# Performance work log

Measured on AMD Instinct MI355X. Metric: run time of the kernel, lower is better.

Reference implementation:

```python
import jax, jax.numpy as jnp
import numpy as np

B, S, D, H, L, V = 2, 1024, 512, 8, 4, 32000
DK = D // H
EPS = 1e-6


def _positional_encoding():
    # row i of the original (d_model, seq) array: sin if i even else cos of t/10000^(2i/D); transposed -> (S, D)
    i = jnp.arange(D, dtype=jnp.float32)
    ang = jnp.arange(S, dtype=jnp.float32)[:, None] / (10000.0 ** (2.0 * i / D))[None, :]
    return jnp.where((jnp.arange(D) % 2 == 0)[None, :], jnp.sin(ang), jnp.cos(ang))


def _layernorm(x, g, b):
    m = jnp.mean(x, axis=-1, keepdims=True)
    s = jnp.std(x, axis=-1, keepdims=True)
    return g / (s + EPS) * (x - m) + b


def _mha(x, wq, wk, wv, wo, mask):
    # wq/wk/wv: [H, D, DK]; all heads batched via einsum (equivalent to per-head loop + concat)
    q = jnp.einsum('bsd,hdk->bhsk', x, wq)
    k = jnp.einsum('bsd,hdk->bhsk', x, wk)
    v = jnp.einsum('bsd,hdk->bhsk', x, wv)
    scores = jnp.einsum('bhsk,bhtk->bhst', q, k) / np.float32(np.sqrt(DK))
    if mask is not None:
        scores = scores + mask  # additive upper-tri 1e-15, faithful to source
    attn = jax.nn.softmax(scores, axis=-1)
    o = jnp.einsum('bhst,bhtv->bhsv', attn, v)
    o = o.transpose(0, 2, 1, 3).reshape(B, S, D)  # concat heads
    return o @ wo


def setup_inputs() -> dict:
    key = jax.random.key(0)
    ks = jax.random.split(key, 13)
    n = lambda k, shape, s=0.05: jax.random.normal(k, shape, dtype=jnp.float32) * s
    return {
        'tokens': jax.random.randint(ks[0], (B, S), 0, V),
        'emb': n(ks[1], (V, D)),
        'Wq': n(ks[2], (L, 2, H, D, DK)),
        'Wk': n(ks[3], (L, 2, H, D, DK)),
        'Wv': n(ks[4], (L, 2, H, D, DK)),
        'Wo': n(ks[5], (L, 2, D, D)),
        'ln_gain': 1.0 + n(ks[6], (L, 3, S, D)),
        'ln_bias': n(ks[7], (L, 3, S, D)),
        'ffn_w1': n(ks[8], (L, D, D)),
        'ffn_b1': n(ks[9], (L, D)),
        'ffn_w2': n(ks[10], (L, D, D)),
        'ffn_b2': n(ks[11], (L, D)),
    }


def reference(tokens, emb, Wq, Wk, Wv, Wo, ln_gain, ln_bias, ffn_w1, ffn_b1, ffn_w2, ffn_b2):
    pe = _positional_encoding()
    # NOTE: source applies sqrt(d_model) scalar AFTER adding positional encoding
    x = (emb[tokens] + pe[None, :, :]) * np.float32(np.sqrt(D))
    # source 'mask' adds 1e-15 to strictly-upper triangle (effectively a no-op; kept faithful)
    mask = (jnp.triu(jnp.ones((S, S), dtype=jnp.float32), 1) * 1e-15)[None, None, :, :]
    for l in range(L):
        h = _mha(x, Wq[l, 0], Wk[l, 0], Wv[l, 0], Wo[l, 0], mask)
        x = _layernorm(x + h, ln_gain[l, 0], ln_bias[l, 0])
        h = _mha(x, Wq[l, 1], Wk[l, 1], Wv[l, 1], Wo[l, 1], None)
        x = _layernorm(x + h, ln_gain[l, 1], ln_bias[l, 1])
        h = jax.nn.relu(x @ ffn_w1[l] + ffn_b1[l]) @ ffn_w2[l] + ffn_b2[l]
        x = _layernorm(x + h, ln_gain[l, 2], ln_bias[l, 2])
    # tied output projection with softmax (SharedWeights on transposed embedding)
    return jax.nn.softmax(x @ emb.T, axis=-1)
```

## Files before the change

kernel.cpp:

```cpp
#include <hip/hip_runtime.h>
#include <hip/hip_bf16.h>

typedef unsigned short u16;
typedef _Float16 f16x8 __attribute__((ext_vector_type(8)));
typedef float f32x4 __attribute__((ext_vector_type(4)));
typedef unsigned short u16x8 __attribute__((ext_vector_type(8)));
typedef unsigned int u32x4 __attribute__((ext_vector_type(4)));

constexpr int kB = 2;
constexpr int kS = 1024;
constexpr int kD = 512;
constexpr int kH = 8;
constexpr int kDK = 64;
constexpr int kL = 4;
constexpr int kV = 32000;
constexpr int kM = kB * kS;
constexpr int kNB = kV / 128;

__device__ __forceinline__ u16 f2fh(float x) {
  _Float16 h = (_Float16)x;
  return __builtin_bit_cast(u16, h);
}
__device__ __forceinline__ float fh2f(u16 h) {
  return (float)__builtin_bit_cast(_Float16, h);
}
__device__ __forceinline__ u16 f2bh(float x) {
  unsigned u = __builtin_bit_cast(unsigned, x);
  unsigned r = u + 0x7fffu + ((u >> 16) & 1u);
  return (u16)(r >> 16);
}
__device__ __forceinline__ float bh2f(u16 h) {
  return __builtin_bit_cast(float, (unsigned)h << 16);
}
__device__ __forceinline__ void gload16(const u16* g, u16* l) {
  __builtin_amdgcn_global_load_lds(
      (const __attribute__((address_space(1))) unsigned int*)g,
      (__attribute__((address_space(3))) unsigned int*)l, 16, 0, 0);
}
__device__ __forceinline__ size_t swz_idx(int row, int k) {
  return (size_t)row * kD + (k & ~63) + ((((k >> 3) & 7) ^ (row & 7)) << 3) + (k & 7);
}

__global__ __launch_bounds__(256)
void conv_qkv(const float* __restrict__ Wq, const float* __restrict__ Wk,
              const float* __restrict__ Wv, u16* __restrict__ oh) {
  __shared__ float ld[64][65];
  const int kc = blockIdx.x, h = blockIdx.y, z = blockIdx.z;
  const int mat = z >> 3, lj = z & 7;
  const float* src = (mat == 0 ? Wq : mat == 1 ? Wk : Wv) +
                     ((size_t)(lj * kH + h)) * kD * kDK + (size_t)kc * 64 * kDK;
  const int t = threadIdx.x;
#pragma unroll
  for (int i = 0; i < 16; ++i) {
    const int idx = i * 256 + t;
    ld[idx >> 6][idx & 63] = src[idx];
  }
  __syncthreads();
  const int dkr = t >> 2, jb = t & 3;
  const size_t rowbase = ((size_t)lj * 1536 + mat * kD + h * kDK + dkr) * kD + kc * 64;
#pragma unroll
  for (int q = 0; q < 2; ++q) {
    const int jj = jb + q * 4;
    const int jsw = jj ^ (dkr & 7);
    u16x8 hi;
#pragma unroll
    for (int e = 0; e < 8; ++e) hi[e] = f2fh(ld[jj * 8 + e][dkr]);
    *(u16x8*)&oh[rowbase + jsw * 8] = hi;
  }
}

__global__ __launch_bounds__(256)
void conv_sq(const float* __restrict__ Wo, const float* __restrict__ w1,
             const float* __restrict__ w2, u16* __restrict__ woh,
             u16* __restrict__ w1h, u16* __restrict__ w2h) {
  __shared__ float ld[64][65];
  const int kc = blockIdx.x, nc = blockIdx.y, mid = blockIdx.z;
  const float* src;
  u16* dh;
  if (mid < 8) { src = Wo + (size_t)mid * kD * kD; dh = woh + (size_t)mid * kD * kD; }
  else if (mid < 12) { int l = mid - 8; src = w1 + (size_t)l * kD * kD; dh = w1h + (size_t)l * kD * kD; }
  else { int l = mid - 12; src = w2 + (size_t)l * kD * kD; dh = w2h + (size_t)l * kD * kD; }
  const int t = threadIdx.x;
#pragma unroll
  for (int i = 0; i < 16; ++i) {
    const int idx = i * 256 + t;
    const int kl = idx >> 6, nl = idx & 63;
    ld[kl][nl] = src[(size_t)(kc * 64 + kl) * kD + nc * 64 + nl];
  }
  __syncthreads();
  const int nr = t >> 2, jb = t & 3;
  const size_t rowbase = (size_t)(nc * 64 + nr) * kD + kc * 64;
#pragma unroll
  for (int q = 0; q < 2; ++q) {
    const int jj = jb + q * 4;
    const int jsw = jj ^ (nr & 7);
    u16x8 hi;
#pragma unroll
    for (int e = 0; e < 8; ++e) hi[e] = f2fh(ld[jj * 8 + e][nr]);
    *(u16x8*)&dh[rowbase + jsw * 8] = hi;
  }
}

__global__ __launch_bounds__(256)
void conv_emb(const float* __restrict__ emb, u16* __restrict__ oh) {
  const int chunk = blockIdx.x * 256 + threadIdx.x;
  const int n = chunk >> 6, j = chunk & 63;
  const float* s = &emb[(size_t)n * kD + j * 8];
  float4 a = *(const float4*)s, b = *(const float4*)(s + 4);
  u16x8 hi;
  hi[0] = f2fh(a.x); hi[1] = f2fh(a.y); hi[2] = f2fh(a.z); hi[3] = f2fh(a.w);
  hi[4] = f2fh(b.x); hi[5] = f2fh(b.y); hi[6] = f2fh(b.z); hi[7] = f2fh(b.w);
  *(u16x8*)&oh[(size_t)n * kD + (j & ~7) * 8 + (((j & 7) ^ (n & 7)) << 3)] = hi;
}

__global__ __launch_bounds__(256)
void conv_gb(const float* __restrict__ g, const float* __restrict__ b,
             unsigned* __restrict__ out) {
  const size_t e0 = ((size_t)blockIdx.x * 256 + threadIdx.x) * 8;
  float4 ga = *(const float4*)&g[e0], gc = *(const float4*)&g[e0 + 4];
  float4 ba = *(const float4*)&b[e0], bc = *(const float4*)&b[e0 + 4];
  u32x4 o0, o1;
  o0[0] = (unsigned)f2fh(ga.x) | ((unsigned)f2fh(ba.x) << 16);
  o0[1] = (unsigned)f2fh(ga.y) | ((unsigned)f2fh(ba.y) << 16);
  o0[2] = (unsigned)f2fh(ga.z) | ((unsigned)f2fh(ba.z) << 16);
  o0[3] = (unsigned)f2fh(ga.w) | ((unsigned)f2fh(ba.w) << 16);
  o1[0] = (unsigned)f2fh(gc.x) | ((unsigned)f2fh(bc.x) << 16);
  o1[1] = (unsigned)f2fh(gc.y) | ((unsigned)f2fh(bc.y) << 16);
  o1[2] = (unsigned)f2fh(gc.z) | ((unsigned)f2fh(bc.z) << 16);
  o1[3] = (unsigned)f2fh(gc.w) | ((unsigned)f2fh(bc.w) << 16);
  *(u32x4*)&out[e0] = o0;
  *(u32x4*)&out[e0 + 4] = o1;
}

__global__ __launch_bounds__(256)
void embed_kernel(const int* __restrict__ tokens, const float* __restrict__ emb,
                  float* __restrict__ x, u16* __restrict__ xh) {
  const int row = blockIdx.x;
  const int s = row & (kS - 1);
  const int tok = tokens[row];
  const float scl = sqrtf((float)kD);
  for (int d = threadIdx.x; d < kD; d += 256) {
    float e = emb[(size_t)tok * kD + d];
    float den = powf(10000.0f, 2.0f * (float)d / (float)kD);
    float ang = (float)s / den;
    float pe = ((d & 1) == 0) ? sinf(ang) : cosf(ang);
    float o = (e + pe) * scl;
    x[(size_t)row * kD + d] = o;
    xh[swz_idx(row, d)] = f2fh(o);
  }
}

template <int BM, int BN, int OUT, int BIAS, int RELU>
__global__ __launch_bounds__(256)
void mgemm2(const u16* __restrict__ Ah, const u16* __restrict__ Bh,
            float* __restrict__ Cf, u16* __restrict__ Ch,
            const float* __restrict__ bias, float* __restrict__ partials,
            int Kd, int Nd) {
  constexpr int MF = BM / 32, NF = BN / 32;
  constexpr int TA = BM * 64;
  constexpr int TB = BN * 64;
  constexpr int BUF = TA + TB;
  __shared__ __align__(16) u16 lds[2 * BUF];
  __shared__ float plds[OUT == 3 ? 2 * BM : 1];
  const int t = threadIdx.x;
  const int lane = t & 63, g = lane >> 4, li = lane & 15;
  const int w = t >> 6, wr = w >> 1, wc = w & 1;
  const int m0 = blockIdx.x * BM, n0 = blockIdx.y * BN;

  f32x4 acc[MF][NF];
#pragma unroll
  for (int i = 0; i < MF; ++i)
#pragma unroll
    for (int j = 0; j < NF; ++j) acc[i][j] = (f32x4){0.f, 0.f, 0.f, 0.f};

  auto stage = [&](int c, int k0) {
    u16* base = &lds[c * BUF];
#pragma unroll
    for (int it = 0; it < (BM * 8) / 256; ++it) {
      const int idx = it * 256 + t;
      gload16(&Ah[(size_t)(m0 + (idx >> 3)) * Kd + k0 + (idx & 7) * 8],
              &base[idx * 8]);
    }
#pragma unroll
    for (int it = 0; it < (BN * 8) / 256; ++it) {
      const int idx = it * 256 + t;
      gload16(&Bh[(size_t)(n0 + (idx >> 3)) * Kd + k0 + (idx & 7) * 8],
              &base[TA + idx * 8]);
    }
  };
  auto compute = [&](int c) {
    const u16* base = &lds[c * BUF];
#pragma unroll
    for (int s = 0; s < 2; ++s) {
      const int s4g = s * 4 + g;
      f16x8 fah[MF], fbh[NF];
#pragma unroll
      for (int fm = 0; fm < MF; ++fm) {
        const int row = wr * (BM / 2) + fm * 16 + li;
        fah[fm] = *(const f16x8*)&base[row * 64 + ((s4g ^ (row & 7)) << 3)];
      }
#pragma unroll
      for (int fn = 0; fn < NF; ++fn) {
        const int row = wc * (BN / 2) + fn * 16 + li;
        fbh[fn] = *(const f16x8*)&base[TA + row * 64 + ((s4g ^ (row & 7)) << 3)];
      }
#pragma unroll
      for (int fm = 0; fm < MF; ++fm)
#pragma unroll
        for (int fn = 0; fn < NF; ++fn)
          acc[fm][fn] = __builtin_amdgcn_mfma_f32_16x16x32_f16(
              fah[fm], fbh[fn], acc[fm][fn], 0, 0, 0);
    }
  };

  stage(0, 0);
  __syncthreads();
  int cur = 0;
  for (int k0 = 64; k0 < Kd; k0 += 64) {
    stage(cur ^ 1, k0);
    compute(cur);
    __syncthreads();
    cur ^= 1;
  }
  compute(cur);

#pragma unroll
  for (int fm = 0; fm < MF; ++fm)
#pragma unroll
    for (int fn = 0; fn < NF; ++fn)
#pragma unroll
      for (int r = 0; r < 4; ++r) {
        const int m = m0 + wr * (BM / 2) + fm * 16 + g * 4 + r;
        const int n = n0 + wc * (BN / 2) + fn * 16 + li;
        float c = acc[fm][fn][r];
        if (BIAS) c += bias[n];
        if (RELU) c = fmaxf(c, 0.0f);
        if (OUT == 0) {
          Cf[(size_t)m * Nd + n] = c;
        } else if (OUT == 1) {
          Ch[swz_idx(m, n)] = f2fh(c);
        } else if (OUT == 2) {
          const int mat = n >> 9, h = (n >> 6) & 7, dk = n & 63;
          const int b_ = m >> 10, s_ = m & (kS - 1);
          Ch[((size_t)mat * kM) * kD +
             (((size_t)(b_ * kH + h) * kS + s_) * kDK + dk)] = f2fh(c);
        } else {
          u16 q = f2bh(__expf(c));
          Ch[(size_t)m * Nd + n] = q;
          acc[fm][fn][r] = bh2f(q);
        }
      }
  if (OUT == 3) {
#pragma unroll
    for (int fm = 0; fm < MF; ++fm)
#pragma unroll
      for (int r = 0; r < 4; ++r) {
        float sv = 0.f;
#pragma unroll
        for (int fn = 0; fn < NF; ++fn) sv += acc[fm][fn][r];
        sv += __shfl_xor(sv, 1); sv += __shfl_xor(sv, 2);
        sv += __shfl_xor(sv, 4); sv += __shfl_xor(sv, 8);
        if (li == 0) plds[wc * BM + wr * (BM / 2) + fm * 16 + g * 4 + r] = sv;
      }
    __syncthreads();
    if (t < BM)
      partials[(size_t)(m0 + t) * gridDim.y + blockIdx.y] = plds[t] + plds[BM + t];
  }
}

__global__ __launch_bounds__(256)
void attn_kernel(const u16* __restrict__ qg, const u16* __restrict__ kg,
                 const u16* __restrict__ vg, u16* __restrict__ aoh) {
  __shared__ __align__(16) u16 Kt[2][2][64][40];
  __shared__ __align__(16) u16 Vt[2][2][64][40];
  __shared__ __align__(16) u16 Pt[2][64][40];
  const int t = threadIdx.x;
  const int lane = t & 63;
  const int g = lane >> 4, li = lane & 15;
  const int w = t >> 6;
  const int bh = blockIdx.y;
  const int q0 = blockIdx.x * 64;
  const size_t base = (size_t)bh * kS * kDK;
  const int r = t >> 2, dq = (t & 3) * 16;

  {
    const u16* src = &qg[base + (size_t)(q0 + r) * kDK + dq];
    u16x8 a = *(const u16x8*)src;
    u16x8 b = *(const u16x8*)(src + 8);
    *(u16x8*)&Pt[dq >> 5][r][dq & 31] = a;
    *(u16x8*)&Pt[dq >> 5][r][(dq & 31) + 8] = b;
  }
  __syncthreads();
  f16x8 qf0 = *(const f16x8*)&Pt[0][w * 16 + li][g * 8];
  f16x8 qf1 = *(const f16x8*)&Pt[1][w * 16 + li][g * 8];
  __syncthreads();

  float m_[4] = {-1e30f, -1e30f, -1e30f, -1e30f};
  float l_[4] = {0.f, 0.f, 0.f, 0.f};
  f32x4 apv[4];
#pragma unroll
  for (int i = 0; i < 4; ++i) apv[i] = (f32x4){0.f, 0.f, 0.f, 0.f};

  u16x8 ka, kb, va, vb;
  auto load_tile = [&](int kt) {
    const u16* ks = &kg[base + (size_t)(kt * 64 + r) * kDK + dq];
    ka = *(const u16x8*)ks;
    kb = *(const u16x8*)(ks + 8);
    const u16* vs = &vg[base + (size_t)(kt * 64 + r) * kDK + dq];
    va = *(const u16x8*)vs;
    vb = *(const u16x8*)(vs + 8);
  };
  auto store_tile = [&](int c) {
    *(u16x8*)&Kt[c][dq >> 5][r][dq & 31] = ka;
    *(u16x8*)&Kt[c][dq >> 5][r][(dq & 31) + 8] = kb;
    const int vc = r >> 5, ko = (r & 31) >> 3, kp = r & 7;
#pragma unroll
    for (int i = 0; i < 8; ++i) {
      const int d = dq + i;
      Vt[c][vc][d][((ko ^ (d >> 4)) << 3) | kp] = va[i];
    }
#pragma unroll
    for (int i = 0; i < 8; ++i) {
      const int d = dq + 8 + i;
      Vt[c][vc][d][((ko ^ (d >> 4)) << 3) | kp] = vb[i];
    }
  };

  load_tile(0);
  store_tile(0);
  for (int kt = 0; kt < kS / 64; ++kt) {
    const int c = kt & 1;
    if (kt < kS / 64 - 1) load_tile(kt + 1);
    __syncthreads();
    f32x4 s[4];
#pragma unroll
    for (int nf = 0; nf < 4; ++nf) {
      f16x8 k0 = *(const f16x8*)&Kt[c][0][nf * 16 + li][g * 8];
      f16x8 k1 = *(const f16x8*)&Kt[c][1][nf * 16 + li][g * 8];
      f32x4 sa = (f32x4){0.f, 0.f, 0.f, 0.f};
      sa = __builtin_amdgcn_mfma_f32_16x16x32_f16(qf0, k0, sa, 0, 0, 0);
      sa = __builtin_amdgcn_mfma_f32_16x16x32_f16(qf1, k1, sa, 0, 0, 0);
      s[nf] = sa;
    }
    float corr[4];
#pragma unroll
    for (int rr = 0; rr < 4; ++rr) {
      float tm = fmaxf(fmaxf(s[0][rr], s[1][rr]), fmaxf(s[2][rr], s[3][rr])) * 0.125f;
      tm = fmaxf(tm, __shfl_xor(tm, 1));
      tm = fmaxf(tm, __shfl_xor(tm, 2));
      tm = fmaxf(tm, __shfl_xor(tm, 4));
      tm = fmaxf(tm, __shfl_xor(tm, 8));
      const float nm = fmaxf(m_[rr], tm);
      corr[rr] = __expf(m_[rr] - nm);
      m_[rr] = nm;
    }
    u16 pb[4][4];
#pragma unroll
    for (int rr = 0; rr < 4; ++rr) {
      float psum = 0.f;
#pragma unroll
      for (int nf = 0; nf < 4; ++nf) {
        float p = __expf(s[nf][rr] * 0.125f - m_[rr]);
        psum += p;
        pb[nf][rr] = f2fh(p);
      }
      l_[rr] = l_[rr] * corr[rr] + psum;
#pragma unroll
      for (int nf = 0; nf < 4; ++nf) apv[nf][rr] *= corr[rr];
    }
#pragma unroll
    for (int nf = 0; nf < 4; ++nf)
#pragma unroll
      for (int rr = 0; rr < 4; ++rr)
        Pt[nf >> 1][w * 16 + g * 4 + rr][(nf & 1) * 16 + li] = pb[nf][rr];
    f16x8 p0 = *(const f16x8*)&Pt[0][w * 16 + li][g * 8];
    f16x8 p1 = *(const f16x8*)&Pt[1][w * 16 + li][g * 8];
#pragma unroll
    for (int nf = 0; nf < 4; ++nf) {
      f16x8 v0 = *(const f16x8*)&Vt[c][0][nf * 16 + li][((g ^ nf) & 3) * 8];
      f16x8 v1 = *(const f16x8*)&Vt[c][1][nf * 16 + li][((g ^ nf) & 3) * 8];
      apv[nf] = __builtin_amdgcn_mfma_f32_16x16x32_f16(p0, v0, apv[nf], 0, 0, 0);
      apv[nf] = __builtin_amdgcn_mfma_f32_16x16x32_f16(p1, v1, apv[nf], 0, 0, 0);
    }
    if (kt < kS / 64 - 1) store_tile(c ^ 1);
  }
#pragma unroll
  for (int rr = 0; rr < 4; ++rr) {
    float ts = l_[rr];
    ts += __shfl_xor(ts, 1); ts += __shfl_xor(ts, 2);
    ts += __shfl_xor(ts, 4); ts += __shfl_xor(ts, 8);
    l_[rr] = ts;
  }
  const int b_ = bh >> 3, h_ = bh & 7;
#pragma unroll
  for (int rr = 0; rr < 4; ++rr) {
    const float inv = 1.0f / l_[rr];
    const int row = q0 + w * 16 + g * 4 + rr;
    const int m = b_ * kS + row;
#pragma unroll
    for (int nf = 0; nf < 4; ++nf) {
      const int d = h_ * kDK + nf * 16 + li;
      aoh[swz_idx(m, d)] = f2fh(apv[nf][rr] * inv);
    }
  }
}

__global__ __launch_bounds__(256)
void ln_kernel(float* __restrict__ x, const float* __restrict__ h,
               const unsigned* __restrict__ gb, u16* __restrict__ xh) {
  const int row = blockIdx.x;
  const int s = row & (kS - 1);
  const int t = threadIdx.x;
  float* xr = x + (size_t)row * kD;
  const float* hr = h + (size_t)row * kD;
  const float v0 = xr[t] + hr[t];
  const float v1 = xr[t + 256] + hr[t + 256];
  float sum = v0 + v1;
  float sq = v0 * v0 + v1 * v1;
#pragma unroll
  for (int off = 1; off < 64; off <<= 1) {
    sum += __shfl_xor(sum, off);
    sq += __shfl_xor(sq, off);
  }
  __shared__ float rs[4], rq[4];
  if ((t & 63) == 0) { rs[t >> 6] = sum; rq[t >> 6] = sq; }
  __syncthreads();
  sum = rs[0] + rs[1] + rs[2] + rs[3];
  sq = rq[0] + rq[1] + rq[2] + rq[3];
  const float mean = sum * (1.0f / kD);
  const float var = fmaxf(sq * (1.0f / kD) - mean * mean, 0.0f);
  const float inv = 1.0f / (sqrtf(var) + 1e-6f);
  const unsigned* gbr = gb + (size_t)s * kD;
  const unsigned p0 = gbr[t], p1 = gbr[t + 256];
  const float o0 = fh2f((u16)p0) * inv * (v0 - mean) + fh2f((u16)(p0 >> 16));
  const float o1 = fh2f((u16)p1) * inv * (v1 - mean) + fh2f((u16)(p1 >> 16));
  xr[t] = o0;
  xr[t + 256] = o1;
  xh[swz_idx(row, t)] = f2fh(o0);
  xh[swz_idx(row, t + 256)] = f2fh(o1);
}

__global__ __launch_bounds__(256)
void scale_kernel(const u16* __restrict__ expb, const float* __restrict__ partials,
                  float* __restrict__ out) {
  const int row = blockIdx.x;
  const int t = threadIdx.x;
  float s = (t < kNB) ? partials[(size_t)row * kNB + t] : 0.f;
#pragma unroll
  for (int off = 1; off < 64; off <<= 1) s += __shfl_xor(s, off);
  __shared__ float red[4];
  if ((t & 63) == 0) red[t >> 6] = s;
  __syncthreads();
  const float inv = 1.0f / (red[0] + red[1] + red[2] + red[3]);
  const u16x8* src = (const u16x8*)(expb + (size_t)row * kV);
  float4* dst = (float4*)(out + (size_t)row * kV);
  for (int i = t; i < kV / 8; i += 256) {
    u16x8 v = src[i];
    float4 a = make_float4(bh2f(v[0]) * inv, bh2f(v[1]) * inv,
                           bh2f(v[2]) * inv, bh2f(v[3]) * inv);
    float4 b = make_float4(bh2f(v[4]) * inv, bh2f(v[5]) * inv,
                           bh2f(v[6]) * inv, bh2f(v[7]) * inv);
    dst[i * 2] = a;
    dst[i * 2 + 1] = b;
  }
}

extern "C" void kernel_launch(void* const* d_in, const int* in_sizes, int n_in,
                              void* d_out, int out_size, void* d_ws, size_t ws_size,
                              hipStream_t stream) {
  (void)in_sizes; (void)n_in; (void)out_size; (void)ws_size;
  const int* tokens = (const int*)d_in[0];
  const float* emb = (const float*)d_in[1];
  const float* Wq = (const float*)d_in[2];
  const float* Wk = (const float*)d_in[3];
  const float* Wv = (const float*)d_in[4];
  const float* Wo = (const float*)d_in[5];
  const float* lng = (const float*)d_in[6];
  const float* lnb = (const float*)d_in[7];
  const float* w1 = (const float*)d_in[8];
  const float* b1 = (const float*)d_in[9];
  const float* w2 = (const float*)d_in[10];
  const float* b2 = (const float*)d_in[11];

  size_t off = 0;
  auto alloc = [&](size_t bytes) {
    void* p = (char*)d_ws + off;
    off += (bytes + 255) & ~(size_t)255;
    return p;
  };
  const size_t NA = (size_t)kM * kD;
  float* x = (float*)alloc(NA * 4);
  u16* xh = (u16*)alloc(NA * 2);
  u16* qkvb = (u16*)alloc(3 * NA * 2);
  u16* aoh = (u16*)alloc(NA * 2);
  float* t1 = (float*)alloc(NA * 4);
  u16* t1h = (u16*)alloc(NA * 2);
  float* ao2 = (float*)alloc(NA * 4);
  float* partials = (float*)alloc((size_t)kM * kNB * 4);
  u16* expb = (u16*)alloc((size_t)kM * kV * 2);
  u16* wqkvh = (u16*)alloc((size_t)8 * 1536 * kD * 2);
  u16* woh = (u16*)alloc((size_t)8 * kD * kD * 2);
  u16* w1h = (u16*)alloc((size_t)4 * kD * kD * 2);
  u16* w2h = (u16*)alloc((size_t)4 * kD * kD * 2);
  u16* embh = (u16*)alloc((size_t)kV * kD * 2);
  unsigned* gb = (unsigned*)alloc((size_t)kL * 3 * kS * kD * 4);

  conv_qkv<<<dim3(8, 8, 24), 256, 0, stream>>>(Wq, Wk, Wv, wqkvh);
  conv_sq<<<dim3(8, 8, 16), 256, 0, stream>>>(Wo, w1, w2, woh, w1h, w2h);
  conv_emb<<<kV * kD / 8 / 256, 256, 0, stream>>>(emb, embh);
  conv_gb<<<kL * 3 * kS * kD / 8 / 256, 256, 0, stream>>>(lng, lnb, gb);
  embed_kernel<<<kM, 256, 0, stream>>>(tokens, emb, x, xh);

  for (int l = 0; l < kL; ++l) {
    for (int j = 0; j < 2; ++j) {
      const size_t lj = (size_t)(l * 2 + j);
      mgemm2<64, 128, 2, 0, 0><<<dim3(kM / 64, 12), 256, 0, stream>>>(
          xh, wqkvh + lj * 1536 * kD, nullptr, qkvb, nullptr, nullptr, kD, 1536);
      attn_kernel<<<dim3(kS / 64, kB * kH), 256, 0, stream>>>(
          qkvb, qkvb + NA, qkvb + 2 * NA, aoh);
      mgemm2<32, 64, 0, 0, 0><<<dim3(kM / 32, kD / 64), 256, 0, stream>>>(
          aoh, woh + lj * kD * kD, t1, nullptr, nullptr, nullptr, kD, kD);
      ln_kernel<<<kM, 256, 0, stream>>>(x, t1, gb + (size_t)(l * 3 + j) * kS * kD, xh);
    }
    mgemm2<32, 64, 1, 1, 1><<<dim3(kM / 32, kD / 64), 256, 0, stream>>>(
        xh, w1h + (size_t)l * kD * kD, nullptr, t1h, b1 + (size_t)l * kD,
        nullptr, kD, kD);
    mgemm2<32, 64, 0, 1, 0><<<dim3(kM / 32, kD / 64), 256, 0, stream>>>(
        t1h, w2h + (size_t)l * kD * kD, ao2, nullptr, b2 + (size_t)l * kD,
        nullptr, kD, kD);
    ln_kernel<<<kM, 256, 0, stream>>>(x, ao2, gb + (size_t)(l * 3 + 2) * kS * kD, xh);
  }
  mgemm2<128, 128, 3, 0, 0><<<dim3(kM / 128, kNB), 256, 0, stream>>>(
      xh, embh, nullptr, expb, nullptr, partials, kD, kV);
  scale_kernel<<<kM, 256, 0, stream>>>(expb, partials, (float*)d_out);
}
```

Measured before the change: 670.2 us.

## Fuse residual-add LayerNorm into the prologue of the following GEMM

The GEMM that follows each LayerNorm (QKV projection or FFN first layer) now computes residual add plus LayerNorm for its BM rows itself and writes the normalized fp16 A tile for the full K into LDS, so only the weight tiles are streamed. The fp32 residual is ping-ponged between two buffers and written only by blocks with blockIdx.y==0, and the final LayerNorm keeps a standalone kernel. This removes 11 of the 12 LN launches and the fp16 activation round trip through global memory. In exchange, every column block recomputes the LayerNorm redundantly, the larger LDS footprint may lower occupancy, and the prologue is serialized before the K loop.

```diff
diff --git a/kernel.cpp b/kernel.cpp
--- a/kernel.cpp
+++ b/kernel.cpp
@@ -150,17 +150,20 @@
   }
 }
 
-template <int BM, int BN, int OUT, int BIAS, int RELU>
+template <int BM, int BN, int OUT, int BIAS, int RELU, int FLN>
 __global__ __launch_bounds__(256)
 void mgemm2(const u16* __restrict__ Ah, const u16* __restrict__ Bh,
             float* __restrict__ Cf, u16* __restrict__ Ch,
             const float* __restrict__ bias, float* __restrict__ partials,
+            const float* __restrict__ Xf, const float* __restrict__ Hf,
+            const unsigned* __restrict__ gbp, float* __restrict__ Xout,
             int Kd, int Nd) {
   constexpr int MF = BM / 32, NF = BN / 32;
   constexpr int TA = BM * 64;
   constexpr int TB = BN * 64;
-  constexpr int BUF = TA + TB;
-  __shared__ __align__(16) u16 lds[2 * BUF];
+  constexpr int ABASE = FLN ? BM * kD : 0;
+  constexpr int LDSU = FLN ? (BM * kD + 2 * TB) : (2 * (TA + TB));
+  __shared__ __align__(16) u16 lds[LDSU];
   __shared__ float plds[OUT == 3 ? 2 * BM : 1];
   const int t = threadIdx.x;
   const int lane = t & 63, g = lane >> 4, li = lane & 15;
@@ -174,22 +177,31 @@
     for (int j = 0; j < NF; ++j) acc[i][j] = (f32x4){0.f, 0.f, 0.f, 0.f};
 
   auto stage = [&](int c, int k0) {
-    u16* base = &lds[c * BUF];
-#pragma unroll
-    for (int it = 0; it < (BM * 8) / 256; ++it) {
-      const int idx = it * 256 + t;
-      gload16(&Ah[(size_t)(m0 + (idx >> 3)) * Kd + k0 + (idx & 7) * 8],
-              &base[idx * 8]);
-    }
-#pragma unroll
-    for (int it = 0; it < (BN * 8) / 256; ++it) {
-      const int idx = it * 256 + t;
-      gload16(&Bh[(size_t)(n0 + (idx >> 3)) * Kd + k0 + (idx & 7) * 8],
-              &base[TA + idx * 8]);
+    if (!FLN) {
+      u16* base = &lds[c * (TA + TB)];
+#pragma unroll
+      for (int it = 0; it < (BM * 8) / 256; ++it) {
+        const int idx = it * 256 + t;
+        gload16(&Ah[(size_t)(m0 + (idx >> 3)) * Kd + k0 + (idx & 7) * 8],
+                &base[idx * 8]);
+      }
+#pragma unroll
+      for (int it = 0; it < (BN * 8) / 256; ++it) {
+        const int idx = it * 256 + t;
+        gload16(&Bh[(size_t)(n0 + (idx >> 3)) * Kd + k0 + (idx & 7) * 8],
+                &base[TA + idx * 8]);
+      }
+    } else {
+      u16* base = &lds[ABASE + c * TB];
+#pragma unroll
+      for (int it = 0; it < (BN * 8) / 256; ++it) {
+        const int idx = it * 256 + t;
+        gload16(&Bh[(size_t)(n0 + (idx >> 3)) * Kd + k0 + (idx & 7) * 8],
+                &base[idx * 8]);
+      }
     }
   };
-  auto compute = [&](int c) {
-    const u16* base = &lds[c * BUF];
+  auto compute = [&](int c, int kp) {
 #pragma unroll
     for (int s = 0; s < 2; ++s) {
       const int s4g = s * 4 + g;
@@ -197,12 +209,17 @@
 #pragma unroll
       for (int fm = 0; fm < MF; ++fm) {
         const int row = wr * (BM / 2) + fm * 16 + li;
-        fah[fm] = *(const f16x8*)&base[row * 64 + ((s4g ^ (row & 7)) << 3)];
-      }
+        if (FLN)
+          fah[fm] = *(const f16x8*)&lds[row * kD + kp + ((s4g ^ (row & 7)) << 3)];
+        else
+          fah[fm] = *(const f16x8*)&lds[c * (TA + TB) + row * 64 +
+                                        ((s4g ^ (row & 7)) << 3)];
+      }
+      const u16* bbase = FLN ? &lds[ABASE + c * TB] : &lds[c * (TA + TB) + TA];
 #pragma unroll
       for (int fn = 0; fn < NF; ++fn) {
         const int row = wc * (BN / 2) + fn * 16 + li;
-        fbh[fn] = *(const f16x8*)&base[TA + row * 64 + ((s4g ^ (row & 7)) << 3)];
+        fbh[fn] = *(const f16x8*)&bbase[row * 64 + ((s4g ^ (row & 7)) << 3)];
       }
 #pragma unroll
       for (int fm = 0; fm < MF; ++fm)
@@ -214,15 +231,71 @@
   };
 
   stage(0, 0);
+  if (FLN) {
+    constexpr int TPR = 256 / BM;
+    constexpr int EPT = kD / TPR;
+    const int rl = t / TPR, part = t % TPR;
+    const int grow = m0 + rl;
+    const float* xr = Xf + (size_t)grow * kD + part * EPT;
+    const float* hr = Hf + (size_t)grow * kD + part * EPT;
+    float sum = 0.f, sq = 0.f;
+    for (int e = 0; e < EPT; e += 4) {
+      float4 xv = *(const float4*)&xr[e];
+      float4 hv = *(const float4*)&hr[e];
+      float a0 = xv.x + hv.x, a1 = xv.y + hv.y;
+      float a2 = xv.z + hv.z, a3 = xv.w + hv.w;
+      sum += (a0 + a1) + (a2 + a3);
+      sq += (a0 * a0 + a1 * a1) + (a2 * a2 + a3 * a3);
+    }
+#pragma unroll
+    for (int off = 1; off < TPR; off <<= 1) {
+      sum += __shfl_xor(sum, off);
+      sq += __shfl_xor(sq, off);
+    }
+    const float mean = sum * (1.0f / kD);
+    const float var = fmaxf(sq * (1.0f / kD) - mean * mean, 0.0f);
+    const float inv = 1.0f / (sqrtf(var) + 1e-6f);
+    const unsigned* gbr = gbp + (size_t)(grow & (kS - 1)) * kD + part * EPT;
+    float* xo = Xout + (size_t)grow * kD + part * EPT;
+    const bool wrx = (blockIdx.y == 0);
+    for (int e = 0; e < EPT; e += 8) {
+      float4 xv = *(const float4*)&xr[e];
+      float4 hv = *(const float4*)&hr[e];
+      float4 xv2 = *(const float4*)&xr[e + 4];
+      float4 hv2 = *(const float4*)&hr[e + 4];
+      u32x4 g0 = *(const u32x4*)&gbr[e];
+      u32x4 g1 = *(const u32x4*)&gbr[e + 4];
+      float o[8];
+      o[0] = fh2f((u16)g0[0]) * inv * (xv.x + hv.x - mean) + fh2f((u16)(g0[0] >> 16));
+      o[1] = fh2f((u16)g0[1]) * inv * (xv.y + hv.y - mean) + fh2f((u16)(g0[1] >> 16));
+      o[2] = fh2f((u16)g0[2]) * inv * (xv.z + hv.z - mean) + fh2f((u16)(g0[2] >> 16));
+      o[3] = fh2f((u16)g0[3]) * inv * (xv.w + hv.w - mean) + fh2f((u16)(g0[3] >> 16));
+      o[4] = fh2f((u16)g1[0]) * inv * (xv2.x + hv2.x - mean) + fh2f((u16)(g1[0] >> 16));
+      o[5] = fh2f((u16)g1[1]) * inv * (xv2.y + hv2.y - mean) + fh2f((u16)(g1[1] >> 16));
+      o[6] = fh2f((u16)g1[2]) * inv * (xv2.z + hv2.z - mean) + fh2f((u16)(g1[2] >> 16));
+      o[7] = fh2f((u16)g1[3]) * inv * (xv2.w + hv2.w - mean) + fh2f((u16)(g1[3] >> 16));
+      u16x8 hbits;
+#pragma unroll
+      for (int i = 0; i < 8; ++i) hbits[i] = f2fh(o[i]);
+      const int k = part * EPT + e;
+      *(u16x8*)&lds[rl * kD + (k & ~63) + (((((k >> 3) & 7)) ^ (rl & 7)) << 3)] =
+          hbits;
+      if (wrx) {
+        *(float4*)&xo[e] = make_float4(o[0], o[1], o[2], o[3]);
+        *(float4*)&xo[e + 4] = make_float4(o[4], o[5], o[6], o[7]);
+      }
+    }
+  }
   __syncthreads();
-  int cur = 0;
+  int cur = 0, kprev = 0;
   for (int k0 = 64; k0 < Kd; k0 += 64) {
     stage(cur ^ 1, k0);
-    compute(cur);
+    compute(cur, kprev);
     __syncthreads();
     cur ^= 1;
-  }
-  compute(cur);
+    kprev = k0;
+  }
+  compute(cur, kprev);
 
 #pragma unroll
   for (int fm = 0; fm < MF; ++fm)
@@ -406,12 +479,12 @@
 }
 
 __global__ __launch_bounds__(256)
-void ln_kernel(float* __restrict__ x, const float* __restrict__ h,
+void ln_kernel(const float* __restrict__ x, const float* __restrict__ h,
                const unsigned* __restrict__ gb, u16* __restrict__ xh) {
   const int row = blockIdx.x;
   const int s = row & (kS - 1);
   const int t = threadIdx.x;
-  float* xr = x + (size_t)row * kD;
+  const float* xr = x + (size_t)row * kD;
   const float* hr = h + (size_t)row * kD;
   const float v0 = xr[t] + hr[t];
   const float v1 = xr[t + 256] + hr[t + 256];
@@ -434,8 +507,6 @@
   const unsigned p0 = gbr[t], p1 = gbr[t + 256];
   const float o0 = fh2f((u16)p0) * inv * (v0 - mean) + fh2f((u16)(p0 >> 16));
   const float o1 = fh2f((u16)p1) * inv * (v1 - mean) + fh2f((u16)(p1 >> 16));
-  xr[t] = o0;
-  xr[t + 256] = o1;
   xh[swz_idx(row, t)] = f2fh(o0);
   xh[swz_idx(row, t + 256)] = f2fh(o1);
 }
@@ -489,7 +560,8 @@
     return p;
   };
   const size_t NA = (size_t)kM * kD;
-  float* x = (float*)alloc(NA * 4);
+  float* xa = (float*)alloc(NA * 4);
+  float* xb = (float*)alloc(NA * 4);
   u16* xh = (u16*)alloc(NA * 2);
   u16* qkvb = (u16*)alloc(3 * NA * 2);
   u16* aoh = (u16*)alloc(NA * 2);
@@ -509,28 +581,48 @@
   conv_sq<<<dim3(8, 8, 16), 256, 0, stream>>>(Wo, w1, w2, woh, w1h, w2h);
   conv_emb<<<kV * kD / 8 / 256, 256, 0, stream>>>(emb, embh);
   conv_gb<<<kL * 3 * kS * kD / 8 / 256, 256, 0, stream>>>(lng, lnb, gb);
-  embed_kernel<<<kM, 256, 0, stream>>>(tokens, emb, x, xh);
+  embed_kernel<<<kM, 256, 0, stream>>>(tokens, emb, xa, xh);
+
+  float* xs[2] = {xa, xb};
+  int cx = 0;
+  const float* fnull = nullptr;
+  const unsigned* unull = nullptr;
 
   for (int l = 0; l < kL; ++l) {
     for (int j = 0; j < 2; ++j) {
       const size_t lj = (size_t)(l * 2 + j);
-      mgemm2<64, 128, 2, 0, 0><<<dim3(kM / 64, 12), 256, 0, stream>>>(
-          xh, wqkvh + lj * 1536 * kD, nullptr, qkvb, nullptr, nullptr, kD, 1536);
+      const u16* wq = wqkvh + lj * 1536 * kD;
+      if (l == 0 && j == 0) {
+        mgemm2<64, 128, 2, 0, 0, 0><<<dim3(kM / 64, 12), 256, 0, stream>>>(
+            xh, wq, nullptr, qkvb, nullptr, nullptr,
+            fnull, fnull, unull, nullptr, kD, 1536);
+      } else {
+        const float* hsrc = (j == 1) ? t1 : ao2;
+        const int gbi = (j == 1) ? (l * 3 + 0) : ((l - 1) * 3 + 2);
+        mgemm2<64, 128, 2, 0, 0, 1><<<dim3(kM / 64, 12), 256, 0, stream>>>(
+            nullptr, wq, nullptr, qkvb, nullptr, nullptr,
+            xs[cx], hsrc, gb + (size_t)gbi * kS * kD, xs[cx ^ 1], kD, 1536);
+        cx ^= 1;
+      }
       attn_kernel<<<dim3(kS / 64, kB * kH), 256, 0, stream>>>(
           qkvb, qkvb + NA, qkvb + 2 * NA, aoh);
-      mgemm2<32, 64, 0, 0, 0><<<dim3(kM / 32, kD / 64), 256, 0, stream>>>(
-          aoh, woh + lj * kD * kD, t1, nullptr, nullptr, nullptr, kD, kD);
-      ln_kernel<<<kM, 256, 0, stream>>>(x, t1, gb + (size_t)(l * 3 + j) * kS * kD, xh);
-    }
-    mgemm2<32, 64, 1, 1, 1><<<dim3(kM / 32, kD / 64), 256, 0, stream>>>(
-        xh, w1h + (size_t)l * kD * kD, nullptr, t1h, b1 + (size_t)l * kD,
-        nullptr, kD, kD);
-    mgemm2<32, 64, 0, 1, 0><<<dim3(kM / 32, kD / 64), 256, 0, stream>>>(
+      mgemm2<32, 64, 0, 0, 0, 0><<<dim3(kM / 32, kD / 64), 256, 0, stream>>>(
+          aoh, woh + lj * kD * kD, t1, nullptr, nullptr, nullptr,
+          fnull, fnull, unull, nullptr, kD, kD);
+    }
+    mgemm2<32, 64, 1, 1, 1, 1><<<dim3(kM / 32, kD / 64), 256, 0, stream>>>(
+        nullptr, w1h + (size_t)l * kD * kD, nullptr, t1h, b1 + (size_t)l * kD,
+        nullptr, xs[cx], t1, gb + (size_t)(l * 3 + 1) * kS * kD, xs[cx ^ 1],
+        kD, kD);
+    cx ^= 1;
+    mgemm2<32, 64, 0, 1, 0, 0><<<dim3(kM / 32, kD / 64), 256, 0, stream>>>(
         t1h, w2h + (size_t)l * kD * kD, ao2, nullptr, b2 + (size_t)l * kD,
-        nullptr, kD, kD);
-    ln_kernel<<<kM, 256, 0, stream>>>(x, ao2, gb + (size_t)(l * 3 + 2) * kS * kD, xh);
-  }
-  mgemm2<128, 128, 3, 0, 0><<<dim3(kM / 128, kNB), 256, 0, stream>>>(
-      xh, embh, nullptr, expb, nullptr, partials, kD, kV);
+        nullptr, fnull, fnull, unull, nullptr, kD, kD);
+  }
+  ln_kernel<<<kM, 256, 0, stream>>>(xs[cx], ao2,
+                                    gb + (size_t)(kL * 3 - 1) * kS * kD, xh);
+  mgemm2<128, 128, 3, 0, 0, 0><<<dim3(kM / 128, kNB), 256, 0, stream>>>(
+      xh, embh, nullptr, expb, nullptr, partials,
+      fnull, fnull, unull, nullptr, kD, kV);
   scale_kernel<<<kM, 256, 0, stream>>>(expb, partials, (float*)d_out);
 }
```

After: 1.031 ms. 1.54x slower.
